# Optimization experiments

Measured on AMD Instinct MI355X. Metric: run time of the kernel, lower is better.

The kernel has to match this reference:

```python
import jax, jax.numpy as jnp
import numpy as np

B, T, DIM = 64, 1, 2048
HQ, HK, D = 16, 4, 128
S_PAST = 4095
EPS = 1e-5
MIN_TS, MAX_TS = 1.0, 10000.0


def setup_inputs() -> dict:
    key = jax.random.key(0)
    ks = jax.random.split(key, 8)
    return {
        "x": jax.random.normal(ks[0], (B, T, DIM), dtype=jnp.float32),
        "pos": jax.random.randint(ks[1], (B, T), 0, S_PAST, dtype=jnp.int64),
        "k_cache": jax.random.normal(ks[2], (B, HK, S_PAST, D), dtype=jnp.float32),
        "v_cache": jax.random.normal(ks[3], (B, HK, S_PAST, D), dtype=jnp.float32),
        "Wq": jax.random.normal(ks[4], (HQ * D, DIM), dtype=jnp.float32) * 0.02,
        "Wk": jax.random.normal(ks[5], (HK * D, DIM), dtype=jnp.float32) * 0.02,
        "Wv": jax.random.normal(ks[6], (HK * D, DIM), dtype=jnp.float32) * 0.02,
        "Wo": jax.random.normal(ks[7], (DIM, HQ * D), dtype=jnp.float32) * 0.02,
        "qn_w": jnp.ones((D,), dtype=jnp.float32),
        "kn_w": jnp.ones((D,), dtype=jnp.float32),
    }


def _rmsnorm(t, w):
    return t * jax.lax.rsqrt(jnp.mean(t * t, axis=-1, keepdims=True) + EPS) * w


def reference(x, pos, k_cache, v_cache, Wq, Wk, Wv, Wo, qn_w, kn_w):
    # projections (fp32), reshape to heads: [B, T, H, D]
    q = (x @ Wq.T).reshape(B, T, HQ, D)
    k = (x @ Wk.T).reshape(B, T, HK, D)
    v = (x @ Wv.T).reshape(B, T, HK, D)

    q = _rmsnorm(q, qn_w)
    k = _rmsnorm(k, kn_w)

    # RoPE: emb built from pos [B, T] -> [B, T, 1, D] broadcast over heads
    half = D // 2
    fraction = 2.0 * jnp.arange(half, dtype=jnp.float32) / D
    inv_freq = 1.0 / (MIN_TS * (MAX_TS / MIN_TS) ** fraction)
    freqs = pos.astype(jnp.float32)[..., None] * inv_freq          # [B, T, half]
    emb = jnp.concatenate([freqs, freqs], axis=-1)[:, :, None, :]   # [B, T, 1, D]
    cos, sin = jnp.cos(emb), jnp.sin(emb)

    def rope(t):
        t1, t2 = jnp.split(t, 2, axis=-1)
        return t * cos + jnp.concatenate([-t2, t1], axis=-1) * sin

    q = rope(q)
    k = rope(k)

    # [B, H, T, D]
    q = q.transpose(0, 2, 1, 3)
    k = k.transpose(0, 2, 1, 3)
    v = v.transpose(0, 2, 1, 3)

    # KV-cache append -> full kv length S_PAST + 1
    kf = jnp.concatenate([k_cache, k], axis=2)  # [B, HK, S+1, D]
    vf = jnp.concatenate([v_cache, v], axis=2)

    # GQA SDPA with scale=1.0 (explicit in the torch module)
    G = HQ // HK
    qg = q.reshape(B, HK, G * T, D)             # group queries under kv heads
    scores = jnp.einsum("bhqd,bhkd->bhqk", qg, kf)
    probs = jax.nn.softmax(scores, axis=-1)
    attn = jnp.einsum("bhqk,bhkd->bhqd", probs, vf)  # [B, HK, G*T, D]
    attn = attn.reshape(B, HQ, T, D).transpose(0, 2, 1, 3).reshape(B, T, HQ * D)

    return attn @ Wo.T  # [B, T, DIM]
```

## Files before the change

kernel.cpp:

```cpp
#include <hip/hip_runtime.h>
#include <math.h>

#define DIM    2048
#define B_     64
#define HQ     16
#define HK     4
#define G_     4
#define D_     128
#define SPAST  4095
#define SEQ    4096
#define NSPLIT 8
#define KSPLIT 4
#define EPS    1e-5f

__global__ __launch_bounds__(256) void gemm64_kernel(
    const float* __restrict__ A,
    const float* __restrict__ W0, const float* __restrict__ W1,
    const float* __restrict__ W2,
    float* __restrict__ part, int N)
{
    const int K  = 2048;
    const int KS = K / KSPLIT;
    int n0 = blockIdx.x * 64;
    int ks = blockIdx.y;
    const float* W; int wc;
    if (n0 < 2048)      { W = W0; wc = n0; }
    else if (n0 < 2560) { W = W1; wc = n0 - 2048; }
    else                { W = W2; wc = n0 - 2560; }

    __shared__ float xt[64][69];
    __shared__ float wt[64][69];

    int t  = threadIdx.x;
    int tx = t & 15, ty = t >> 4;
    float acc[4][4] = {};

    int k0 = ks * KS;
    for (int kc = k0; kc < k0 + KS; kc += 64) {
        __syncthreads();
        #pragma unroll
        for (int r = 0; r < 4; ++r) {
            int bi = ty + r * 16;
            float4 xv = *(const float4*)&A[(size_t)bi * K + kc + tx * 4];
            xt[tx*4+0][bi] = xv.x; xt[tx*4+1][bi] = xv.y;
            xt[tx*4+2][bi] = xv.z; xt[tx*4+3][bi] = xv.w;
            float4 wv = *(const float4*)&W[(size_t)(wc + bi) * K + kc + tx * 4];
            wt[tx*4+0][bi] = wv.x; wt[tx*4+1][bi] = wv.y;
            wt[tx*4+2][bi] = wv.z; wt[tx*4+3][bi] = wv.w;
        }
        __syncthreads();
        #pragma unroll 8
        for (int k = 0; k < 64; ++k) {
            float xr[4], wr[4];
            #pragma unroll
            for (int i = 0; i < 4; ++i) xr[i] = xt[k][ty*4+i];
            #pragma unroll
            for (int j = 0; j < 4; ++j) wr[j] = wt[k][tx*4+j];
            #pragma unroll
            for (int i = 0; i < 4; ++i)
                #pragma unroll
                for (int j = 0; j < 4; ++j)
                    acc[i][j] += xr[i] * wr[j];
        }
    }
    #pragma unroll
    for (int i = 0; i < 4; ++i)
        #pragma unroll
        for (int j = 0; j < 4; ++j)
            part[((size_t)ks * 64 + ty*4+i) * N + n0 + tx*4 + j] = acc[i][j];
}

__global__ __launch_bounds__(256) void rope_norm_kernel(
    const float* __restrict__ part1, const int* __restrict__ pos,
    const float* __restrict__ qn_w, const float* __restrict__ kn_w,
    float* __restrict__ qr, float* __restrict__ kr, float* __restrict__ vr)
{
    int row  = blockIdx.x * 4 + (threadIdx.x >> 6);
    int lane = threadIdx.x & 63;
    int b = row / 24, h = row % 24;
    int col, type;
    if (h < 16)      { type = 0; col = h * 128; }
    else if (h < 20) { type = 1; col = 2048 + (h - 16) * 128; }
    else             { type = 2; col = 2560 + (h - 20) * 128; }

    float t1 = 0.f, t2 = 0.f;
    #pragma unroll
    for (int ksp = 0; ksp < KSPLIT; ++ksp) {
        t1 += part1[((size_t)ksp * 64 + b) * 3072 + col + lane];
        t2 += part1[((size_t)ksp * 64 + b) * 3072 + col + lane + 64];
    }

    if (type == 2) {
        vr[(b * HK + (h - 20)) * 128 + lane]      = t1;
        vr[(b * HK + (h - 20)) * 128 + lane + 64] = t2;
        return;
    }

    float ss = t1 * t1 + t2 * t2;
    ss += __shfl_xor(ss, 1);  ss += __shfl_xor(ss, 2);  ss += __shfl_xor(ss, 4);
    ss += __shfl_xor(ss, 8);  ss += __shfl_xor(ss, 16); ss += __shfl_xor(ss, 32);
    float rn = 1.0f / sqrtf(ss * (1.0f / 128.0f) + EPS);
    const float* wn = (type == 0) ? qn_w : kn_w;
    float n1 = t1 * rn * wn[lane];
    float n2 = t2 * rn * wn[lane + 64];

    float invf = powf(10000.0f, -(float)lane * (1.0f / 64.0f));
    float f    = (float)pos[b] * invf;
    float sv = sinf(f), cv = cosf(f);
    float o1 = n1 * cv - n2 * sv;
    float o2 = n2 * cv + n1 * sv;

    if (type == 0) {
        qr[(b * HQ + h) * 128 + lane]      = o1;
        qr[(b * HQ + h) * 128 + lane + 64] = o2;
    } else {
        kr[(b * HK + (h - 16)) * 128 + lane]      = o1;
        kr[(b * HK + (h - 16)) * 128 + lane + 64] = o2;
    }
}

__global__ __launch_bounds__(256) void attn_kernel(
    const float* __restrict__ kc, const float* __restrict__ vc,
    const float* __restrict__ qr, const float* __restrict__ kr,
    const float* __restrict__ vr,
    float* __restrict__ pacc, float* __restrict__ pml)
{
    int blk  = blockIdx.x;
    int sp   = blk & (NSPLIT - 1);
    int hk   = (blk / NSPLIT) & (HK - 1);
    int b    = blk / (NSPLIT * HK);
    int t    = threadIdx.x;
    int w    = t >> 6;
    int lane = t & 63;
    int half = (lane >> 5) & 1;
    int l32  = lane & 31;
    int g    = lane & 3;
    int dbase = (l32 >> 2) * 16;

    float4 q4[G_];
    #pragma unroll
    for (int gg = 0; gg < G_; ++gg)
        q4[gg] = *(const float4*)&qr[(size_t)(b * HQ + hk * G_ + gg) * D_ + l32 * 4];

    const float* kbase = kc + (size_t)(b * HK + hk) * SPAST * D_;
    const float* vbase = vc + (size_t)(b * HK + hk) * SPAST * D_;
    const float* knew  = kr + (b * HK + hk) * D_;
    const float* vnew  = vr + (b * HK + hk) * D_;

    float  m = -1e30f, lsum = 0.f;
    float4 acc[4];
    #pragma unroll
    for (int j = 0; j < 4; ++j) acc[j] = make_float4(0.f, 0.f, 0.f, 0.f);

    int s0 = sp * (SEQ / NSPLIT);
    int s  = s0 + w * 2 + half;
    const float* kp = (s < SPAST) ? (kbase + (size_t)s * D_) : knew;
    float4 k4 = *(const float4*)(kp + l32 * 4);

    int sel1 = lane & 1, sel2 = lane & 2;

    for (int i = 0; i < 64; ++i) {
        const float* vp = (s < SPAST) ? (vbase + (size_t)s * D_) : vnew;
        float4 v4[4];
        #pragma unroll
        for (int j = 0; j < 4; ++j)
            v4[j] = *(const float4*)(vp + dbase + j * 4);

        float4 k4n;
        int sn = s;
        if (i < 63) {
            sn = s0 + ((i + 1) * 4 + w) * 2 + half;
            const float* kpn = (sn < SPAST) ? (kbase + (size_t)sn * D_) : knew;
            k4n = *(const float4*)(kpn + l32 * 4);
        }

        float p0 = q4[0].x*k4.x + q4[0].y*k4.y + q4[0].z*k4.z + q4[0].w*k4.w;
        float p1 = q4[1].x*k4.x + q4[1].y*k4.y + q4[1].z*k4.z + q4[1].w*k4.w;
        float p2 = q4[2].x*k4.x + q4[2].y*k4.y + q4[2].z*k4.z + q4[2].w*k4.w;
        float p3 = q4[3].x*k4.x + q4[3].y*k4.y + q4[3].z*k4.z + q4[3].w*k4.w;

        float ka = sel1 ? p1 : p0, sa = sel1 ? p0 : p1;
        float kb = sel1 ? p3 : p2, sb = sel1 ? p2 : p3;
        float s01 = ka + __shfl_xor(sa, 1);
        float s23 = kb + __shfl_xor(sb, 1);
        float kc2 = sel2 ? s23 : s01, sc = sel2 ? s01 : s23;
        float p = kc2 + __shfl_xor(sc, 2);
        p += __shfl_xor(p, 4);
        p += __shfl_xor(p, 8);
        p += __shfl_xor(p, 16);

        if (p > m + 8.0f) {
            float al = __expf(m - p);
            m = p;
            lsum *= al;
            #pragma unroll
            for (int j = 0; j < 4; ++j) {
                acc[j].x *= al; acc[j].y *= al; acc[j].z *= al; acc[j].w *= al;
            }
        }
        float e = __expf(p - m);
        lsum += e;
        #pragma unroll
        for (int j = 0; j < 4; ++j) {
            acc[j].x += e * v4[j].x; acc[j].y += e * v4[j].y;
            acc[j].z += e * v4[j].z; acc[j].w += e * v4[j].w;
        }

        k4 = k4n; s = sn;
    }

    __shared__ float s_acc[8][G_][D_];
    __shared__ float s_m[8][G_];
    __shared__ float s_l[8][G_];
    int wh = w * 2 + half;
    #pragma unroll
    for (int j = 0; j < 4; ++j)
        *(float4*)&s_acc[wh][g][dbase + j * 4] = acc[j];
    if (l32 < 4) { s_m[wh][l32] = m; s_l[wh][l32] = lsum; }
    __syncthreads();

    if (t < 128) {
        int d = t;
        #pragma unroll
        for (int gg = 0; gg < G_; ++gg) {
            float M = -1e30f;
            #pragma unroll
            for (int j = 0; j < 8; ++j) M = fmaxf(M, s_m[j][gg]);
            float L = 0.f, a = 0.f;
            #pragma unroll
            for (int j = 0; j < 8; ++j) {
                float e = __expf(s_m[j][gg] - M);
                L += e * s_l[j][gg];
                a += e * s_acc[j][gg][d];
            }
            int hq = hk * G_ + gg;
            size_t pidx = (size_t)(b * HQ + hq) * NSPLIT + sp;
            pacc[pidx * D_ + d] = a;
            if (d == 0) { pml[pidx * 2 + 0] = M; pml[pidx * 2 + 1] = L; }
        }
    }
}

__global__ void attn_combine_kernel(const float* __restrict__ pacc,
                                    const float* __restrict__ pml,
                                    float* __restrict__ attnb)
{
    int bh = blockIdx.x;
    int d  = threadIdx.x;
    float M = -1e30f;
    #pragma unroll
    for (int s = 0; s < NSPLIT; ++s)
        M = fmaxf(M, pml[(size_t)(bh * NSPLIT + s) * 2]);
    float L = 0.f, a = 0.f;
    #pragma unroll
    for (int s = 0; s < NSPLIT; ++s) {
        float e = __expf(pml[(size_t)(bh * NSPLIT + s) * 2] - M);
        L += e * pml[(size_t)(bh * NSPLIT + s) * 2 + 1];
        a += e * pacc[(size_t)(bh * NSPLIT + s) * D_ + d];
    }
    attnb[(size_t)bh * D_ + d] = a / L;
}

__global__ void sum_parts_kernel(const float* __restrict__ part,
                                 float* __restrict__ out)
{
    int i = blockIdx.x * 256 + threadIdx.x;
    float v = 0.f;
    #pragma unroll
    for (int ksp = 0; ksp < KSPLIT; ++ksp)
        v += part[(size_t)ksp * B_ * DIM + i];
    out[i] = v;
}

extern "C" void kernel_launch(void* const* d_in, const int* in_sizes, int n_in,
                              void* d_out, int out_size, void* d_ws, size_t ws_size,
                              hipStream_t stream)
{
    const float* x   = (const float*)d_in[0];
    const int*   pos = (const int*)  d_in[1];
    const float* kc  = (const float*)d_in[2];
    const float* vc  = (const float*)d_in[3];
    const float* Wq  = (const float*)d_in[4];
    const float* Wk  = (const float*)d_in[5];
    const float* Wv  = (const float*)d_in[6];
    const float* Wo  = (const float*)d_in[7];
    const float* qn  = (const float*)d_in[8];
    const float* kn  = (const float*)d_in[9];

    float* ws    = (float*)d_ws;
    float* part1 = ws;
    float* qr    = part1 + (size_t)KSPLIT * 64 * 3072;
    float* kr    = qr    + (size_t)64 * HQ * D_;
    float* vr    = kr    + (size_t)64 * HK * D_;
    float* pacc  = vr    + (size_t)64 * HK * D_;
    float* pml   = pacc  + (size_t)64 * HQ * NSPLIT * D_;
    float* attnb = pml   + (size_t)64 * HQ * NSPLIT * 2;
    float* part4 = attnb + (size_t)64 * DIM;

    gemm64_kernel<<<dim3(48, KSPLIT), 256, 0, stream>>>(x, Wq, Wk, Wv, part1, 3072);
    rope_norm_kernel<<<384, 256, 0, stream>>>(part1, pos, qn, kn, qr, kr, vr);
    attn_kernel<<<B_ * HK * NSPLIT, 256, 0, stream>>>(kc, vc, qr, kr, vr, pacc, pml);
    attn_combine_kernel<<<B_ * HQ, 128, 0, stream>>>(pacc, pml, attnb);
    gemm64_kernel<<<dim3(32, KSPLIT), 256, 0, stream>>>(attnb, Wo, Wo, Wo, part4, 2048);
    sum_parts_kernel<<<(B_ * DIM) / 256, 256, 0, stream>>>(part4, (float*)d_out);
}
```

Before: 261.1 us.

## Double-buffer K/V loads in attention with nontemporal loads and doubled GEMM K-split

The attention loop now prefetches both K and V for the next step instead of only K, and uses nontemporal loads for the streaming cache reads. The final iteration is peeled so the new-token boundary check runs once rather than on every step. It also adds an occupancy hint to the attention kernel's launch bounds and raises the GEMM K-split from 4 to 8. The aim is more memory-level parallelism on the bandwidth-bound KV stream, at the cost of more registers per thread and more partial-sum traffic in the GEMM.

```diff
diff --git a/kernel.cpp b/kernel.cpp
--- a/kernel.cpp
+++ b/kernel.cpp
@@ -10,8 +10,10 @@
 #define SPAST  4095
 #define SEQ    4096
 #define NSPLIT 8
-#define KSPLIT 4
+#define KSPLIT 8
 #define EPS    1e-5f
+
+typedef float f4 __attribute__((ext_vector_type(4)));
 
 __global__ __launch_bounds__(256) void gemm64_kernel(
     const float* __restrict__ A,
@@ -119,7 +121,7 @@
     }
 }
 
-__global__ __launch_bounds__(256) void attn_kernel(
+__global__ __launch_bounds__(256, 4) void attn_kernel(
     const float* __restrict__ kc, const float* __restrict__ vc,
     const float* __restrict__ qr, const float* __restrict__ kr,
     const float* __restrict__ vr,
@@ -127,58 +129,36 @@
 {
     int blk  = blockIdx.x;
     int sp   = blk & (NSPLIT - 1);
-    int hk   = (blk / NSPLIT) & (HK - 1);
-    int b    = blk / (NSPLIT * HK);
+    int hk   = (blk >> 3) & (HK - 1);
+    int b    = blk >> 5;
     int t    = threadIdx.x;
-    int w    = t >> 6;
-    int lane = t & 63;
-    int half = (lane >> 5) & 1;
-    int l32  = lane & 31;
-    int g    = lane & 3;
+    int wh   = t >> 5;
+    int l32  = t & 31;
+    int g    = t & 3;
     int dbase = (l32 >> 2) * 16;
-
-    float4 q4[G_];
+    int sel1 = l32 & 1, sel2 = l32 & 2;
+
+    const float* qrb = qr + (size_t)(b * HQ + hk * G_) * D_;
+    f4 q4[G_];
     #pragma unroll
     for (int gg = 0; gg < G_; ++gg)
-        q4[gg] = *(const float4*)&qr[(size_t)(b * HQ + hk * G_ + gg) * D_ + l32 * 4];
+        q4[gg] = *(const f4*)&qrb[gg * D_ + l32 * 4];
 
     const float* kbase = kc + (size_t)(b * HK + hk) * SPAST * D_;
     const float* vbase = vc + (size_t)(b * HK + hk) * SPAST * D_;
     const float* knew  = kr + (b * HK + hk) * D_;
     const float* vnew  = vr + (b * HK + hk) * D_;
 
-    float  m = -1e30f, lsum = 0.f;
-    float4 acc[4];
-    #pragma unroll
-    for (int j = 0; j < 4; ++j) acc[j] = make_float4(0.f, 0.f, 0.f, 0.f);
-
-    int s0 = sp * (SEQ / NSPLIT);
-    int s  = s0 + w * 2 + half;
-    const float* kp = (s < SPAST) ? (kbase + (size_t)s * D_) : knew;
-    float4 k4 = *(const float4*)(kp + l32 * 4);
-
-    int sel1 = lane & 1, sel2 = lane & 2;
-
-    for (int i = 0; i < 64; ++i) {
-        const float* vp = (s < SPAST) ? (vbase + (size_t)s * D_) : vnew;
-        float4 v4[4];
-        #pragma unroll
-        for (int j = 0; j < 4; ++j)
-            v4[j] = *(const float4*)(vp + dbase + j * 4);
-
-        float4 k4n;
-        int sn = s;
-        if (i < 63) {
-            sn = s0 + ((i + 1) * 4 + w) * 2 + half;
-            const float* kpn = (sn < SPAST) ? (kbase + (size_t)sn * D_) : knew;
-            k4n = *(const float4*)(kpn + l32 * 4);
-        }
-
-        float p0 = q4[0].x*k4.x + q4[0].y*k4.y + q4[0].z*k4.z + q4[0].w*k4.w;
-        float p1 = q4[1].x*k4.x + q4[1].y*k4.y + q4[1].z*k4.z + q4[1].w*k4.w;
-        float p2 = q4[2].x*k4.x + q4[2].y*k4.y + q4[2].z*k4.z + q4[2].w*k4.w;
-        float p3 = q4[3].x*k4.x + q4[3].y*k4.y + q4[3].z*k4.z + q4[3].w*k4.w;
-
+    float m = -1e30f, lsum = 0.f;
+    f4 acc[4];
+    #pragma unroll
+    for (int j = 0; j < 4; ++j) acc[j] = (f4)0.f;
+
+    auto COMPUTE = [&](const f4& k4, const f4* v4) {
+        float p0 = q4[0][0]*k4[0] + q4[0][1]*k4[1] + q4[0][2]*k4[2] + q4[0][3]*k4[3];
+        float p1 = q4[1][0]*k4[0] + q4[1][1]*k4[1] + q4[1][2]*k4[2] + q4[1][3]*k4[3];
+        float p2 = q4[2][0]*k4[0] + q4[2][1]*k4[1] + q4[2][2]*k4[2] + q4[2][3]*k4[3];
+        float p3 = q4[3][0]*k4[0] + q4[3][1]*k4[1] + q4[3][2]*k4[2] + q4[3][3]*k4[3];
         float ka = sel1 ? p1 : p0, sa = sel1 ? p0 : p1;
         float kb = sel1 ? p3 : p2, sb = sel1 ? p2 : p3;
         float s01 = ka + __shfl_xor(sa, 1);
@@ -188,34 +168,60 @@
         p += __shfl_xor(p, 4);
         p += __shfl_xor(p, 8);
         p += __shfl_xor(p, 16);
-
         if (p > m + 8.0f) {
             float al = __expf(m - p);
             m = p;
             lsum *= al;
             #pragma unroll
-            for (int j = 0; j < 4; ++j) {
-                acc[j].x *= al; acc[j].y *= al; acc[j].z *= al; acc[j].w *= al;
-            }
+            for (int j = 0; j < 4; ++j) acc[j] *= al;
         }
         float e = __expf(p - m);
         lsum += e;
         #pragma unroll
-        for (int j = 0; j < 4; ++j) {
-            acc[j].x += e * v4[j].x; acc[j].y += e * v4[j].y;
-            acc[j].z += e * v4[j].z; acc[j].w += e * v4[j].w;
-        }
-
-        k4 = k4n; s = sn;
+        for (int j = 0; j < 4; ++j) acc[j] += e * v4[j];
+    };
+
+    int off_k = (sp * 512 + wh) * D_ + l32 * 4;
+    int off_v = (sp * 512 + wh) * D_ + dbase;
+
+    f4 k4 = __builtin_nontemporal_load((const f4*)(kbase + off_k));
+    f4 v4[4];
+    #pragma unroll
+    for (int j = 0; j < 4; ++j)
+        v4[j] = __builtin_nontemporal_load((const f4*)(vbase + off_v + j * 4));
+
+    for (int i = 0; i < 62; ++i) {
+        off_k += 8 * D_; off_v += 8 * D_;
+        f4 k4n = __builtin_nontemporal_load((const f4*)(kbase + off_k));
+        f4 v4n[4];
+        #pragma unroll
+        for (int j = 0; j < 4; ++j)
+            v4n[j] = __builtin_nontemporal_load((const f4*)(vbase + off_v + j * 4));
+        COMPUTE(k4, v4);
+        k4 = k4n;
+        #pragma unroll
+        for (int j = 0; j < 4; ++j) v4[j] = v4n[j];
+    }
+    COMPUTE(k4, v4);
+
+    {
+        int s_f = sp * 512 + 504 + wh;
+        const float* kp = (s_f < SPAST) ? (kbase + (size_t)s_f * D_ + l32 * 4)
+                                        : (knew + l32 * 4);
+        const float* vp = (s_f < SPAST) ? (vbase + (size_t)s_f * D_ + dbase)
+                                        : (vnew + dbase);
+        k4 = *(const f4*)kp;
+        #pragma unroll
+        for (int j = 0; j < 4; ++j) v4[j] = *(const f4*)(vp + j * 4);
+        COMPUTE(k4, v4);
     }
 
     __shared__ float s_acc[8][G_][D_];
     __shared__ float s_m[8][G_];
     __shared__ float s_l[8][G_];
-    int wh = w * 2 + half;
     #pragma unroll
     for (int j = 0; j < 4; ++j)
-        *(float4*)&s_acc[wh][g][dbase + j * 4] = acc[j];
+        *(f4*)&s_acc[wh][g][dbase + j * 4] = acc[j];
     if (l32 < 4) { s_m[wh][l32] = m; s_l[wh][l32] = lsum; }
     __syncthreads();
 
```

Measured after the change: 276.7 us. 1.06x slower.

## Use bf16 MFMA for projection GEMMs and double the K-split

Applied to the files above, without the earlier changes.

Replaces the scalar fp32 LDS-tiled GEMM with a kernel that converts A and W tiles to bf16 on load, stores them in swizzled LDS, and runs mfma_f32_16x16x32_bf16. KSPLIT rises from 4 to 8 so more blocks run per GEMM. The aim is to cut the FMA-bound projection and output GEMM time, at the cost of bf16 rounding of fp32 inputs and a larger partial-sum buffer to reduce. The workspace offsets and the rope and sum kernels loop over KSPLIT, so the buffer sizes follow the new value.

```diff
diff --git a/kernel.cpp b/kernel.cpp
--- a/kernel.cpp
+++ b/kernel.cpp
@@ -10,10 +10,18 @@
 #define SPAST  4095
 #define SEQ    4096
 #define NSPLIT 8
-#define KSPLIT 4
+#define KSPLIT 8
 #define EPS    1e-5f
 
-__global__ __launch_bounds__(256) void gemm64_kernel(
+typedef short bfrag __attribute__((ext_vector_type(8)));
+typedef float facc  __attribute__((ext_vector_type(4)));
+
+__device__ inline unsigned short f2bf(float f) {
+    unsigned u = __float_as_uint(f);
+    return (unsigned short)((u + 0x7FFFu + ((u >> 16) & 1u)) >> 16);
+}
+
+__global__ __launch_bounds__(256) void gemm_mfma_kernel(
     const float* __restrict__ A,
     const float* __restrict__ W0, const float* __restrict__ W1,
     const float* __restrict__ W2,
@@ -28,46 +36,73 @@
     else if (n0 < 2560) { W = W1; wc = n0 - 2048; }
     else                { W = W2; wc = n0 - 2560; }
 
-    __shared__ float xt[64][69];
-    __shared__ float wt[64][69];
-
-    int t  = threadIdx.x;
-    int tx = t & 15, ty = t >> 4;
-    float acc[4][4] = {};
-
-    int k0 = ks * KS;
-    for (int kc = k0; kc < k0 + KS; kc += 64) {
+    __shared__ bfrag a_lds[64 * 8];
+    __shared__ bfrag w_lds[64 * 8];
+
+    int t = threadIdx.x;
+    int w = t >> 6, l = t & 63;
+    int row_s = t >> 2;
+    int q_s   = t & 3;
+    int sw_s  = row_s & 7;
+    int c0    = q_s * 2;
+
+    facc acc[4] = {};
+
+    const float* Abase = A + (size_t)row_s * K + (size_t)ks * KS + q_s * 16;
+    const float* Wbase = W + (size_t)(wc + row_s) * K + (size_t)ks * KS + q_s * 16;
+
+    for (int kt = 0; kt < KS; kt += 64) {
         __syncthreads();
+        {
+            const float* p = Abase + kt;
+            float4 f0 = *(const float4*)(p);
+            float4 f1 = *(const float4*)(p + 4);
+            float4 f2 = *(const float4*)(p + 8);
+            float4 f3 = *(const float4*)(p + 12);
+            bfrag v0, v1;
+            v0[0]=f2bf(f0.x); v0[1]=f2bf(f0.y); v0[2]=f2bf(f0.z); v0[3]=f2bf(f0.w);
+            v0[4]=f2bf(f1.x); v0[5]=f2bf(f1.y); v0[6]=f2bf(f1.z); v0[7]=f2bf(f1.w);
+            v1[0]=f2bf(f2.x); v1[1]=f2bf(f2.y); v1[2]=f2bf(f2.z); v1[3]=f2bf(f2.w);
+            v1[4]=f2bf(f3.x); v1[5]=f2bf(f3.y); v1[6]=f2bf(f3.z); v1[7]=f2bf(f3.w);
+            a_lds[row_s * 8 + ((c0    ) ^ sw_s)] = v0;
+            a_lds[row_s * 8 + ((c0 + 1) ^ sw_s)] = v1;
+        }
+        {
+            const float* p = Wbase + kt;
+            float4 f0 = *(const float4*)(p);
+            float4 f1 = *(const float4*)(p + 4);
+            float4 f2 = *(const float4*)(p + 8);
+            float4 f3 = *(const float4*)(p + 12);
+            bfrag v0, v1;
+            v0[0]=f2bf(f0.x); v0[1]=f2bf(f0.y); v0[2]=f2bf(f0.z); v0[3]=f2bf(f0.w);
+            v0[4]=f2bf(f1.x); v0[5]=f2bf(f1.y); v0[6]=f2bf(f1.z); v0[7]=f2bf(f1.w);
+            v1[0]=f2bf(f2.x); v1[1]=f2bf(f2.y); v1[2]=f2bf(f2.z); v1[3]=f2bf(f2.w);
+            v1[4]=f2bf(f3.x); v1[5]=f2bf(f3.y); v1[6]=f2bf(f3.z); v1[7]=f2bf(f3.w);
+            w_lds[row_s * 8 + ((c0    ) ^ sw_s)] = v0;
+            w_lds[row_s * 8 + ((c0 + 1) ^ sw_s)] = v1;
+        }
+        __syncthreads();
+        #pragma unroll
+        for (int kc = 0; kc < 2; ++kc) {
+            int nrow = w * 16 + (l & 15);
+            bfrag bf = w_lds[nrow * 8 + ((kc * 4 + (l >> 4)) ^ (nrow & 7))];
+            #pragma unroll
+            for (int rg = 0; rg < 4; ++rg) {
+                int arow = rg * 16 + (l & 15);
+                bfrag af = a_lds[arow * 8 + ((kc * 4 + (l >> 4)) ^ (arow & 7))];
+                acc[rg] = __builtin_amdgcn_mfma_f32_16x16x32_bf16(af, bf, acc[rg], 0, 0, 0);
+            }
+        }
+    }
+    #pragma unroll
+    for (int rg = 0; rg < 4; ++rg) {
         #pragma unroll
         for (int r = 0; r < 4; ++r) {
-            int bi = ty + r * 16;
-            float4 xv = *(const float4*)&A[(size_t)bi * K + kc + tx * 4];
-            xt[tx*4+0][bi] = xv.x; xt[tx*4+1][bi] = xv.y;
-            xt[tx*4+2][bi] = xv.z; xt[tx*4+3][bi] = xv.w;
-            float4 wv = *(const float4*)&W[(size_t)(wc + bi) * K + kc + tx * 4];
-            wt[tx*4+0][bi] = wv.x; wt[tx*4+1][bi] = wv.y;
-            wt[tx*4+2][bi] = wv.z; wt[tx*4+3][bi] = wv.w;
-        }
-        __syncthreads();
-        #pragma unroll 8
-        for (int k = 0; k < 64; ++k) {
-            float xr[4], wr[4];
-            #pragma unroll
-            for (int i = 0; i < 4; ++i) xr[i] = xt[k][ty*4+i];
-            #pragma unroll
-            for (int j = 0; j < 4; ++j) wr[j] = wt[k][tx*4+j];
-            #pragma unroll
-            for (int i = 0; i < 4; ++i)
-                #pragma unroll
-                for (int j = 0; j < 4; ++j)
-                    acc[i][j] += xr[i] * wr[j];
-        }
-    }
-    #pragma unroll
-    for (int i = 0; i < 4; ++i)
-        #pragma unroll
-        for (int j = 0; j < 4; ++j)
-            part[((size_t)ks * 64 + ty*4+i) * N + n0 + tx*4 + j] = acc[i][j];
+            int row = rg * 16 + (l >> 4) * 4 + r;
+            int col = n0 + w * 16 + (l & 15);
+            part[((size_t)ks * 64 + row) * N + col] = acc[rg][r];
+        }
+    }
 }
 
 __global__ __launch_bounds__(256) void rope_norm_kernel(
@@ -127,8 +162,8 @@
 {
     int blk  = blockIdx.x;
     int sp   = blk & (NSPLIT - 1);
-    int hk   = (blk / NSPLIT) & (HK - 1);
-    int b    = blk / (NSPLIT * HK);
+    int hk   = (blk >> 3) & (HK - 1);
+    int b    = blk >> 5;
     int t    = threadIdx.x;
     int w    = t >> 6;
     int lane = t & 63;
@@ -136,6 +171,7 @@
     int l32  = lane & 31;
     int g    = lane & 3;
     int dbase = (l32 >> 2) * 16;
+    int sel1 = lane & 1, sel2 = lane & 2;
 
     float4 q4[G_];
     #pragma unroll
@@ -156,8 +192,6 @@
     int s  = s0 + w * 2 + half;
     const float* kp = (s < SPAST) ? (kbase + (size_t)s * D_) : knew;
     float4 k4 = *(const float4*)(kp + l32 * 4);
-
-    int sel1 = lane & 1, sel2 = lane & 2;
 
     for (int i = 0; i < 64; ++i) {
         const float* vp = (s < SPAST) ? (vbase + (size_t)s * D_) : vnew;
@@ -297,10 +331,10 @@
     float* attnb = pml   + (size_t)64 * HQ * NSPLIT * 2;
     float* part4 = attnb + (size_t)64 * DIM;
 
-    gemm64_kernel<<<dim3(48, KSPLIT), 256, 0, stream>>>(x, Wq, Wk, Wv, part1, 3072);
+    gemm_mfma_kernel<<<dim3(48, KSPLIT), 256, 0, stream>>>(x, Wq, Wk, Wv, part1, 3072);
     rope_norm_kernel<<<384, 256, 0, stream>>>(part1, pos, qn, kn, qr, kr, vr);
     attn_kernel<<<B_ * HK * NSPLIT, 256, 0, stream>>>(kc, vc, qr, kr, vr, pacc, pml);
     attn_combine_kernel<<<B_ * HQ, 128, 0, stream>>>(pacc, pml, attnb);
-    gemm64_kernel<<<dim3(32, KSPLIT), 256, 0, stream>>>(attnb, Wo, Wo, Wo, part4, 2048);
+    gemm_mfma_kernel<<<dim3(32, KSPLIT), 256, 0, stream>>>(attnb, Wo, Wo, Wo, part4, 2048);
     sum_parts_kernel<<<(B_ * DIM) / 256, 256, 0, stream>>>(part4, (float*)d_out);
 }
```

Result: faster. 226.4 us (-13.3%).
